# Optimization experiments

Hardware: AMD Instinct MI355X
Metric: run time of the kernel (lower is better)

## Reference

```python
import jax, jax.numpy as jnp
import numpy as np

HIDDEN = 768
HEADS = 12
HEAD_DIM = HIDDEN // HEADS
LN_EPS = 1e-12


def setup_inputs() -> dict:
    key = jax.random.key(0)
    ks = jax.random.split(key, 12)
    B, Lq, Lk = 8, 512, 1024
    s = 0.02
    return {
        "query": jax.random.normal(ks[0], (B, Lq, HIDDEN), jnp.float32),
        "key": jax.random.normal(ks[1], (B, Lk, HIDDEN), jnp.float32),
        "value": jax.random.normal(ks[2], (B, Lk, HIDDEN), jnp.float32),
        "attention_mask": jnp.zeros((B, 1, 1, Lk), jnp.float32),
        "q_attention_mask": jnp.zeros((B, 1, 1, Lq), jnp.float32),
        "Wq": jax.random.normal(ks[3], (HIDDEN, HIDDEN), jnp.float32) * s,
        "bq": jnp.zeros((HIDDEN,), jnp.float32),
        "Wk": jax.random.normal(ks[4], (HIDDEN, HIDDEN), jnp.float32) * s,
        "bk": jnp.zeros((HIDDEN,), jnp.float32),
        "Wv": jax.random.normal(ks[5], (HIDDEN, HIDDEN), jnp.float32) * s,
        "bv": jnp.zeros((HIDDEN,), jnp.float32),
        "Wo": jax.random.normal(ks[6], (HIDDEN, HIDDEN), jnp.float32) * s,
        "bo": jnp.zeros((HIDDEN,), jnp.float32),
        "ln_gamma": jnp.ones((HIDDEN,), jnp.float32),
        "ln_beta": jnp.zeros((HIDDEN,), jnp.float32),
    }


def _split_heads(x):  # [B, L, H*D] -> [B, H, L, D]
    B, L, _ = x.shape
    return x.reshape(B, L, HEADS, HEAD_DIM).transpose(0, 2, 1, 3)


def reference(query, key, value, attention_mask, q_attention_mask,
              Wq, bq, Wk, bk, Wv, bv, Wo, bo, ln_gamma, ln_beta):
    # QKV projections (dropout is identity at inference)
    q = _split_heads(query @ Wq.T + bq)   # [B,H,Lq,D]
    k = _split_heads(key @ Wk.T + bk)     # [B,H,Lk,D]
    v = _split_heads(value @ Wv.T + bv)   # [B,H,Lk,D]

    scores = jnp.einsum("bhqd,bhkd->bhqk", q, k) / jnp.sqrt(
        jnp.asarray(HEAD_DIM, q.dtype))
    scores = scores + attention_mask  # additive mask broadcast [B,1,1,Lk]
    probs = jax.nn.softmax(scores, axis=-1)
    ctx = jnp.einsum("bhqk,bhkd->bhqd", probs, v)  # [B,H,Lq,D]
    B, H, Lq, D = ctx.shape
    ctx = ctx.transpose(0, 2, 1, 3).reshape(B, Lq, H * D)

    # BertSelfOutput: dense + residual + LayerNorm
    h = ctx @ Wo.T + bo + query
    mu = jnp.mean(h, axis=-1, keepdims=True)
    var = jnp.mean(jnp.square(h - mu), axis=-1, keepdims=True)
    out = (h - mu) / jnp.sqrt(var + LN_EPS) * ln_gamma + ln_beta
    return out, probs
```

## Files before the change

kernel.cpp:

```cpp
#include <hip/hip_runtime.h>
#include <math.h>

#define HIDDEN 768
#define NHEADS 12
#define DHEAD  64
#define NB     8
#define LQ     512
#define LK     1024
#define LN_EPS 1e-12f
#define TS     1032

typedef __attribute__((ext_vector_type(8))) short short8;
typedef __attribute__((ext_vector_type(4))) float floatx4;

#define GLDS16(gp, lp) __builtin_amdgcn_global_load_lds( \
    (const __attribute__((address_space(1))) void*)(gp), \
    (__attribute__((address_space(3))) void*)(lp), 16, 0, 0)

__device__ __forceinline__ short f2bf(float f) {
    unsigned u = __float_as_uint(f);
    u = u + 0x7FFFu + ((u >> 16) & 1u);
    return (short)(u >> 16);
}

__device__ __forceinline__ float bf2f(short s) {
    return __uint_as_float(((unsigned)(unsigned short)s) << 16);
}

__global__ __launch_bounds__(256)
void cvt_f32_bf16(const float* __restrict__ in, short* __restrict__ out, int n4)
{
    int i = blockIdx.x * 256 + threadIdx.x;
    if (i >= n4) return;
    float4 v = ((const float4*)in)[i];
    short4 o;
    o.x = f2bf(v.x); o.y = f2bf(v.y); o.z = f2bf(v.z); o.w = f2bf(v.w);
    ((short4*)out)[i] = o;
}

__global__ __launch_bounds__(256)
void gemm_nt_mfma(const short* __restrict__ A, const short* __restrict__ B,
                  float* __restrict__ Cf, short* __restrict__ Cb,
                  const float* __restrict__ bias, const float* __restrict__ res,
                  int K, int lda, int ldb, int ldc, float alpha)
{
    __shared__ short As[4096];
    __shared__ short Bs[4096];

    int n0 = blockIdx.x * 128;
    int m0 = blockIdx.y * 128;
    int t    = threadIdx.x;
    int lane = t & 63, wave = t >> 6;
    int quad = lane >> 4, l15 = lane & 15;
    int wr = wave >> 1, wc = wave & 1;

    int e0 = t, e1 = 256 + t;
    int r0 = e0 >> 2, c0 = (e0 & 3) ^ ((r0 >> 1) & 3);
    int r1 = e1 >> 2, c1 = (e1 & 3) ^ ((r1 >> 1) & 3);
    const short* Ap0 = A + (size_t)(m0 + r0) * lda + c0 * 8;
    const short* Ap1 = A + (size_t)(m0 + r1) * lda + c1 * 8;
    const short* Bp0 = B + (size_t)(n0 + r0) * ldb + c0 * 8;
    const short* Bp1 = B + (size_t)(n0 + r1) * ldb + c1 * 8;

    int aoff[4], boff[4];
#pragma unroll
    for (int i = 0; i < 4; i++) {
        int ra = wr * 64 + i * 16 + l15;
        aoff[i] = (ra * 4 + (quad ^ ((ra >> 1) & 3))) * 8;
        int rb = wc * 64 + i * 16 + l15;
        boff[i] = (rb * 4 + (quad ^ ((rb >> 1) & 3))) * 8;
    }

    floatx4 acc[4][4] = {};

    for (int k0 = 0; k0 < K; k0 += 32) {
        GLDS16(Ap0, &As[e0 * 8]);
        GLDS16(Ap1, &As[e1 * 8]);
        GLDS16(Bp0, &Bs[e0 * 8]);
        GLDS16(Bp1, &Bs[e1 * 8]);
        Ap0 += 32; Ap1 += 32; Bp0 += 32; Bp1 += 32;
        __syncthreads();

        short8 af[4], bfr[4];
#pragma unroll
        for (int i = 0; i < 4; i++) af[i]  = *(const short8*)&As[aoff[i]];
#pragma unroll
        for (int j = 0; j < 4; j++) bfr[j] = *(const short8*)&Bs[boff[j]];
#pragma unroll
        for (int i = 0; i < 4; i++)
#pragma unroll
            for (int j = 0; j < 4; j++)
                acc[i][j] = __builtin_amdgcn_mfma_f32_16x16x32_bf16(
                    af[i], bfr[j], acc[i][j], 0, 0, 0);
        __syncthreads();
    }

#pragma unroll
    for (int i = 0; i < 4; i++) {
        int mb = m0 + wr * 64 + i * 16 + quad * 4;
#pragma unroll
        for (int j = 0; j < 4; j++) {
            int n = n0 + wc * 64 + j * 16 + l15;
            float bv = bias ? bias[n] : 0.f;
#pragma unroll
            for (int r = 0; r < 4; r++) {
                int m = mb + r;
                float v = alpha * acc[i][j][r] + bv;
                if (res) v += res[(size_t)m * ldc + n];
                if (Cb) Cb[(size_t)m * ldc + n] = f2bf(v);
                else    Cf[(size_t)m * ldc + n] = v;
            }
        }
    }
}

__global__ __launch_bounds__(256)
void transpose_v(const short* __restrict__ vb, short* __restrict__ vt)
{
    __shared__ short T[256 * 72];
    int kt = blockIdx.x, bh = blockIdx.y;
    int b = bh / 12, h = bh - b * 12;
    int t = threadIdx.x;
    const short* src = vb + ((size_t)b * LK + kt * 256) * HIDDEN + h * DHEAD;
#pragma unroll
    for (int it = 0; it < 8; it++) {
        int s = it * 256 + t;
        int k = s >> 3, c = s & 7;
        *(short8*)&T[k * 72 + c * 8] =
            *(const short8*)&src[(size_t)k * HIDDEN + c * 8];
    }
    __syncthreads();
    short* dst = vt + (size_t)bh * DHEAD * LK + kt * 256;
#pragma unroll
    for (int it = 0; it < 8; it++) {
        int s = it * 256 + t;
        int d = s >> 5, kc = s & 31;
        short8 v;
#pragma unroll
        for (int i = 0; i < 8; i++) v[i] = T[(kc * 8 + i) * 72 + d];
        *(short8*)&dst[(size_t)d * LK + kc * 8] = v;
    }
}

__global__ __launch_bounds__(256)
void fused_attn(const short* __restrict__ qb, const short* __restrict__ kb,
                const short* __restrict__ vt, const float* __restrict__ amask,
                float* __restrict__ probs, short* __restrict__ ctxb)
{
    __shared__ short S[16 * TS];
    __shared__ short KV[8192];
    __shared__ float mpart[4][16];
    __shared__ float lrow[16];

    int flat = blockIdx.y * 32 + blockIdx.x;
    int jj   = flat >> 3;
    int bh   = (flat & 7) * 12 + jj % 12;
    int qt   = jj / 12;
    int b = bh / 12, h = bh - b * 12;
    int m0 = qt * 16;

    const short* Qg = qb + ((size_t)b * LQ + m0) * HIDDEN + h * DHEAD;
    const short* Kg = kb + (size_t)b * LK * HIDDEN + h * DHEAD;
    const short* Vg = vt + (size_t)bh * DHEAD * LK;
    const float* Mg = amask + (size_t)b * LK;
    float* Pg = probs + (size_t)bh * LQ * LK + (size_t)m0 * LK;
    short* Cg = ctxb + ((size_t)b * LQ + m0) * HIDDEN + h * DHEAD;

    int t = threadIdx.x;
    int lane = t & 63, w = t >> 6;
    int quad = lane >> 4, l15 = lane & 15;

#pragma unroll
    for (int I = 0; I < 4; I++) {
        int s = I * 256 + t;
        int r = s >> 3, cs = s & 7, c = cs ^ (r & 7);
        GLDS16(Kg + (size_t)r * HIDDEN + c * 8, &KV[s * 8]);
    }

    short8 af[2];
#pragma unroll
    for (int ks = 0; ks < 2; ks++)
        af[ks] = *(const short8*)&Qg[(size_t)l15 * HIDDEN + ks * 32 + quad * 8];

    float mx[4];
#pragma unroll
    for (int r = 0; r < 4; r++) mx[r] = -3.0e38f;

    const float SC  = 0.125f * 1.44269504089f;
    const float L2E = 1.44269504089f;

    for (int kc = 0; kc < 8; kc++) {
        __syncthreads();
        floatx4 acc[2] = {};
#pragma unroll
        for (int ks = 0; ks < 2; ks++)
#pragma unroll
            for (int j = 0; j < 2; j++) {
                int rK = w * 32 + j * 16 + l15;
                int cs = (ks * 4 + quad) ^ (rK & 7);
                short8 bfr = *(const short8*)&KV[(rK * 8 + cs) * 8];
                acc[j] = __builtin_amdgcn_mfma_f32_16x16x32_bf16(
                    af[ks], bfr, acc[j], 0, 0, 0);
            }
        __syncthreads();
        if (kc < 7) {
            const short* Kn = Kg + (size_t)(kc + 1) * 128 * HIDDEN;
#pragma unroll
            for (int I = 0; I < 4; I++) {
                int s = I * 256 + t;
                int r = s >> 3, cs = s & 7, c = cs ^ (r & 7);
                GLDS16(Kn + (size_t)r * HIDDEN + c * 8, &KV[s * 8]);
            }
        }
#pragma unroll
        for (int j = 0; j < 2; j++) {
            int n = kc * 128 + w * 32 + j * 16 + l15;
            float mk = Mg[n] * L2E;
#pragma unroll
            for (int r = 0; r < 4; r++) {
                int m = quad * 4 + r;
                float v = acc[j][r] * SC + mk;
                S[m * TS + n] = f2bf(v);
                mx[r] = fmaxf(mx[r], v);
            }
        }
    }

#pragma unroll
    for (int d = 1; d < 16; d <<= 1)
#pragma unroll
        for (int r = 0; r < 4; r++)
            mx[r] = fmaxf(mx[r], __shfl_xor(mx[r], d));
    if (l15 == 0)
#pragma unroll
        for (int r = 0; r < 4; r++)
            mpart[w][quad * 4 + r] = mx[r];
    __syncthreads();

#pragma unroll
    for (int I = 0; I < 4; I++) {
        int s = I * 256 + t;
        int n = s >> 4, cs = s & 15, c = cs ^ (n & 15);
        GLDS16(Vg + (size_t)n * LK + c * 8, &KV[s * 8]);
    }

    {
        int r = t >> 4, seg = t & 15;
        float mr = fmaxf(fmaxf(mpart[0][r], mpart[1][r]),
                         fmaxf(mpart[2][r], mpart[3][r]));
        float sum = 0.f;
#pragma unroll
        for (int i = 0; i < 8; i++) {
            int u = i * 16 + seg;
            short8 v = *(const short8*)&S[r * TS + u * 8];
            short8 o;
#pragma unroll
            for (int e = 0; e < 8; e++) {
                float f = exp2f(bf2f(v[e]) - mr);
                o[e] = f2bf(f);
                sum += f;
            }
            *(short8*)&S[r * TS + u * 8] = o;
        }
        sum += __shfl_xor(sum, 1);
        sum += __shfl_xor(sum, 2);
        sum += __shfl_xor(sum, 4);
        sum += __shfl_xor(sum, 8);
        if (seg == 0) lrow[r] = sum;
    }

    floatx4 accO = {};
    for (int kc = 0; kc < 8; kc++) {
        __syncthreads();
#pragma unroll
        for (int ks = 0; ks < 4; ks++) {
            short8 pa = *(const short8*)&S[l15 * TS + kc * 128
                                           + ks * 32 + quad * 8];
            int n = w * 16 + l15;
            int cs = (ks * 4 + quad) ^ (n & 15);
            short8 bfr = *(const short8*)&KV[(n * 16 + cs) * 8];
            accO = __builtin_amdgcn_mfma_f32_16x16x32_bf16(
                pa, bfr, accO, 0, 0, 0);
        }
        __syncthreads();
        if (kc < 7) {
            const short* Vn = Vg + (kc + 1) * 128;
#pragma unroll
            for (int I = 0; I < 4; I++) {
                int s = I * 256 + t;
                int n = s >> 4, cs = s & 15, c = cs ^ (n & 15);
                GLDS16(Vn + (size_t)n * LK + c * 8, &KV[s * 8]);
            }
        }
#pragma unroll
        for (int rr = 0; rr < 2; rr++) {
            int r = kc * 2 + rr;
            float inv = 1.0f / lrow[r];
            short4 v = *(const short4*)&S[r * TS + t * 4];
            floatx4 o;
            o.x = bf2f(v.x) * inv; o.y = bf2f(v.y) * inv;
            o.z = bf2f(v.z) * inv; o.w = bf2f(v.w) * inv;
            __builtin_nontemporal_store(
                o, (floatx4*)(Pg + (size_t)r * LK) + t);
        }
    }

    int n = w * 16 + l15;
#pragma unroll
    for (int r = 0; r < 4; r++) {
        int m = quad * 4 + r;
        Cg[(size_t)m * HIDDEN + n] = f2bf(accO[r] / lrow[m]);
    }
}

__global__ __launch_bounds__(256)
void layernorm_rows(const float* __restrict__ H, const float* __restrict__ gamma,
                    const float* __restrict__ beta, float* __restrict__ out)
{
    int row = blockIdx.x;
    const float* h = H + (long)row * HIDDEN;
    int t = threadIdx.x;

    float x[3];
    float s = 0.f, ss = 0.f;
#pragma unroll
    for (int i = 0; i < 3; i++) {
        x[i] = h[t + 256 * i];
        s  += x[i];
        ss += x[i] * x[i];
    }
#pragma unroll
    for (int off = 32; off > 0; off >>= 1) {
        s  += __shfl_down(s, off);
        ss += __shfl_down(ss, off);
    }
    __shared__ float sh_s[4], sh_ss[4];
    int wave = t >> 6;
    if ((t & 63) == 0) { sh_s[wave] = s; sh_ss[wave] = ss; }
    __syncthreads();
    float S  = sh_s[0] + sh_s[1] + sh_s[2] + sh_s[3];
    float SS = sh_ss[0] + sh_ss[1] + sh_ss[2] + sh_ss[3];

    float mu  = S * (1.0f / HIDDEN);
    float var = SS * (1.0f / HIDDEN) - mu * mu;
    float inv = rsqrtf(var + LN_EPS);

    float* o = out + (long)row * HIDDEN;
#pragma unroll
    for (int i = 0; i < 3; i++) {
        int c = t + 256 * i;
        o[c] = (x[i] - mu) * inv * gamma[c] + beta[c];
    }
}

extern "C" void kernel_launch(void* const* d_in, const int* in_sizes, int n_in,
                              void* d_out, int out_size, void* d_ws, size_t ws_size,
                              hipStream_t stream)
{
    const float* query = (const float*)d_in[0];
    const float* key   = (const float*)d_in[1];
    const float* value = (const float*)d_in[2];
    const float* amask = (const float*)d_in[3];
    const float* Wq    = (const float*)d_in[5];
    const float* bq    = (const float*)d_in[6];
    const float* Wk    = (const float*)d_in[7];
    const float* bk    = (const float*)d_in[8];
    const float* Wv    = (const float*)d_in[9];
    const float* bv    = (const float*)d_in[10];
    const float* Wo    = (const float*)d_in[11];
    const float* bo    = (const float*)d_in[12];
    const float* gamma = (const float*)d_in[13];
    const float* beta  = (const float*)d_in[14];

    short* qx = (short*)d_ws;
    short* kx = qx + (long)4096 * 768;
    short* vx = kx + (long)8192 * 768;
    short* wq = vx + (long)8192 * 768;
    short* wk = wq + (long)768 * 768;
    short* wv = wk + (long)768 * 768;
    short* wo = wv + (long)768 * 768;
    short* qb = wo + (long)768 * 768;
    short* kb = qb + (long)4096 * 768;
    short* vb = kb + (long)8192 * 768;
    short* ctxb = qx;
    short* vt   = kx;
    float* hbuf = (float*)vx;

    float* out0  = (float*)d_out;
    float* probs = out0 + (long)NB * LQ * HIDDEN;

    cvt_f32_bf16<<<(4096 * 768 / 4 + 255) / 256, 256, 0, stream>>>(query, qx, 4096 * 768 / 4);
    cvt_f32_bf16<<<(8192 * 768 / 4 + 255) / 256, 256, 0, stream>>>(key,   kx, 8192 * 768 / 4);
    cvt_f32_bf16<<<(8192 * 768 / 4 + 255) / 256, 256, 0, stream>>>(value, vx, 8192 * 768 / 4);
    cvt_f32_bf16<<<(768 * 768 / 4 + 255) / 256, 256, 0, stream>>>(Wq, wq, 768 * 768 / 4);
    cvt_f32_bf16<<<(768 * 768 / 4 + 255) / 256, 256, 0, stream>>>(Wk, wk, 768 * 768 / 4);
    cvt_f32_bf16<<<(768 * 768 / 4 + 255) / 256, 256, 0, stream>>>(Wv, wv, 768 * 768 / 4);
    cvt_f32_bf16<<<(768 * 768 / 4 + 255) / 256, 256, 0, stream>>>(Wo, wo, 768 * 768 / 4);

    gemm_nt_mfma<<<dim3(6, 32), 256, 0, stream>>>(
        qx, wq, nullptr, qb, bq, nullptr, HIDDEN, HIDDEN, HIDDEN, HIDDEN, 1.0f);
    gemm_nt_mfma<<<dim3(6, 64), 256, 0, stream>>>(
        kx, wk, nullptr, kb, bk, nullptr, HIDDEN, HIDDEN, HIDDEN, HIDDEN, 1.0f);
    gemm_nt_mfma<<<dim3(6, 64), 256, 0, stream>>>(
        vx, wv, nullptr, vb, bv, nullptr, HIDDEN, HIDDEN, HIDDEN, HIDDEN, 1.0f);

    transpose_v<<<dim3(4, 96), 256, 0, stream>>>(vb, vt);

    fused_attn<<<dim3(32, 96), 256, 0, stream>>>(qb, kb, vt, amask, probs, ctxb);

    gemm_nt_mfma<<<dim3(6, 32), 256, 0, stream>>>(
        ctxb, wo, hbuf, nullptr, bo, query, HIDDEN, HIDDEN, HIDDEN, HIDDEN, 1.0f);

    layernorm_rows<<<NB * LQ, 256, 0, stream>>>(hbuf, gamma, beta, out0);
}
```

Before: 476.5 us.

## Merge conversion and QKV GEMM launches, double-buffer GEMM LDS loads

All seven fp32-to-bf16 conversions now run in one launch, and the three QKV projection GEMMs run in one grid that dispatches per block-row. The GEMM core now double-buffers its LDS tiles, issuing the next K-step's global-to-LDS loads before the current step's MFMAs and dropping one barrier per iteration. This cuts launch overhead, fills the device better for the small Q GEMM, and overlaps memory with compute. The cost is doubled LDS per block, which may lower occupancy, and a single barrier per step, which relies on the async-load ordering being safe.

```diff
diff --git a/kernel.cpp b/kernel.cpp
--- a/kernel.cpp
+++ b/kernel.cpp
@@ -28,27 +28,40 @@
 }
 
 __global__ __launch_bounds__(256)
-void cvt_f32_bf16(const float* __restrict__ in, short* __restrict__ out, int n4)
-{
-    int i = blockIdx.x * 256 + threadIdx.x;
-    if (i >= n4) return;
-    float4 v = ((const float4*)in)[i];
+void cvt_all(const float* __restrict__ q, const float* __restrict__ k,
+             const float* __restrict__ v,
+             const float* __restrict__ Wq, const float* __restrict__ Wk,
+             const float* __restrict__ Wv, const float* __restrict__ Wo,
+             short* __restrict__ dq, short* __restrict__ dk,
+             short* __restrict__ dv,
+             short* __restrict__ dwq, short* __restrict__ dwk,
+             short* __restrict__ dwv, short* __restrict__ dwo)
+{
+    int bx = blockIdx.x;
+    const float* src; short* dst; int base;
+    if (bx < 3072)       { src = q; dst = dq; base = bx; }
+    else if (bx < 9216)  { src = k; dst = dk; base = bx - 3072; }
+    else if (bx < 15360) { src = v; dst = dv; base = bx - 9216; }
+    else {
+        int wb = bx - 15360, wsel = wb / 576;
+        base = wb - wsel * 576;
+        src = (wsel == 0) ? Wq : (wsel == 1) ? Wk : (wsel == 2) ? Wv : Wo;
+        dst = (wsel == 0) ? dwq : (wsel == 1) ? dwk : (wsel == 2) ? dwv : dwo;
+    }
+    int i = base * 256 + threadIdx.x;
+    float4 vv = ((const float4*)src)[i];
     short4 o;
-    o.x = f2bf(v.x); o.y = f2bf(v.y); o.z = f2bf(v.z); o.w = f2bf(v.w);
-    ((short4*)out)[i] = o;
-}
-
-__global__ __launch_bounds__(256)
-void gemm_nt_mfma(const short* __restrict__ A, const short* __restrict__ B,
-                  float* __restrict__ Cf, short* __restrict__ Cb,
-                  const float* __restrict__ bias, const float* __restrict__ res,
-                  int K, int lda, int ldb, int ldc, float alpha)
-{
-    __shared__ short As[4096];
-    __shared__ short Bs[4096];
-
-    int n0 = blockIdx.x * 128;
-    int m0 = blockIdx.y * 128;
+    o.x = f2bf(vv.x); o.y = f2bf(vv.y); o.z = f2bf(vv.z); o.w = f2bf(vv.w);
+    ((short4*)dst)[i] = o;
+}
+
+__device__ __forceinline__ void gemm_core(
+    short (*As)[4096], short (*Bs)[4096],
+    const short* __restrict__ A, const short* __restrict__ B,
+    float* Cf, short* Cb,
+    const float* bias, const float* res,
+    int m0, int n0, int K, int lda, int ldb, int ldc, float alpha)
+{
     int t    = threadIdx.x;
     int lane = t & 63, wave = t >> 6;
     int quad = lane >> 4, l15 = lane & 15;
@@ -72,27 +85,35 @@
     }
 
     floatx4 acc[4][4] = {};
-
-    for (int k0 = 0; k0 < K; k0 += 32) {
-        GLDS16(Ap0, &As[e0 * 8]);
-        GLDS16(Ap1, &As[e1 * 8]);
-        GLDS16(Bp0, &Bs[e0 * 8]);
-        GLDS16(Bp1, &Bs[e1 * 8]);
-        Ap0 += 32; Ap1 += 32; Bp0 += 32; Bp1 += 32;
+    int nsteps = K >> 5;
+
+    GLDS16(Ap0, &As[0][e0 * 8]);
+    GLDS16(Ap1, &As[0][e1 * 8]);
+    GLDS16(Bp0, &Bs[0][e0 * 8]);
+    GLDS16(Bp1, &Bs[0][e1 * 8]);
+    Ap0 += 32; Ap1 += 32; Bp0 += 32; Bp1 += 32;
+
+    for (int s = 0; s < nsteps; s++) {
+        int cur = s & 1;
         __syncthreads();
-
+        if (s + 1 < nsteps) {
+            GLDS16(Ap0, &As[cur ^ 1][e0 * 8]);
+            GLDS16(Ap1, &As[cur ^ 1][e1 * 8]);
+            GLDS16(Bp0, &Bs[cur ^ 1][e0 * 8]);
+            GLDS16(Bp1, &Bs[cur ^ 1][e1 * 8]);
+            Ap0 += 32; Ap1 += 32; Bp0 += 32; Bp1 += 32;
+        }
         short8 af[4], bfr[4];
 #pragma unroll
-        for (int i = 0; i < 4; i++) af[i]  = *(const short8*)&As[aoff[i]];
-#pragma unroll
-        for (int j = 0; j < 4; j++) bfr[j] = *(const short8*)&Bs[boff[j]];
+        for (int i = 0; i < 4; i++) af[i]  = *(const short8*)&As[cur][aoff[i]];
+#pragma unroll
+        for (int j = 0; j < 4; j++) bfr[j] = *(const short8*)&Bs[cur][boff[j]];
 #pragma unroll
         for (int i = 0; i < 4; i++)
 #pragma unroll
             for (int j = 0; j < 4; j++)
                 acc[i][j] = __builtin_amdgcn_mfma_f32_16x16x32_bf16(
                     af[i], bfr[j], acc[i][j], 0, 0, 0);
-        __syncthreads();
     }
 
 #pragma unroll
@@ -112,6 +133,39 @@
             }
         }
     }
+}
+
+__global__ __launch_bounds__(256)
+void gemm_nt_mfma(const short* __restrict__ A, const short* __restrict__ B,
+                  float* __restrict__ Cf, short* __restrict__ Cb,
+                  const float* __restrict__ bias, const float* __restrict__ res,
+                  int K, int lda, int ldb, int ldc, float alpha)
+{
+    __shared__ short As[2][4096];
+    __shared__ short Bs[2][4096];
+    gemm_core(As, Bs, A, B, Cf, Cb, bias, res,
+              blockIdx.y * 128, blockIdx.x * 128, K, lda, ldb, ldc, alpha);
+}
+
+__global__ __launch_bounds__(256)
+void qkv_gemm(const short* __restrict__ qx, const short* __restrict__ kx,
+              const short* __restrict__ vx,
+              const short* __restrict__ wq, const short* __restrict__ wk,
+              const short* __restrict__ wv,
+              const float* __restrict__ bq, const float* __restrict__ bk,
+              const float* __restrict__ bv,
+              short* __restrict__ qb, short* __restrict__ kb,
+              short* __restrict__ vb)
+{
+    __shared__ short As[2][4096];
+    __shared__ short Bs[2][4096];
+    int yb = blockIdx.y;
+    const short *A, *B; const float* bias; short* C; int m0;
+    if (yb < 32)      { A = qx; B = wq; bias = bq; C = qb; m0 = yb * 128; }
+    else if (yb < 96) { A = kx; B = wk; bias = bk; C = kb; m0 = (yb - 32) * 128; }
+    else              { A = vx; B = wv; bias = bv; C = vb; m0 = (yb - 96) * 128; }
+    gemm_core(As, Bs, A, B, nullptr, C, bias, nullptr,
+              m0, blockIdx.x * 128, HIDDEN, HIDDEN, HIDDEN, HIDDEN, 1.0f);
 }
 
 __global__ __launch_bounds__(256)
@@ -389,20 +443,11 @@
     float* out0  = (float*)d_out;
     float* probs = out0 + (long)NB * LQ * HIDDEN;
 
-    cvt_f32_bf16<<<(4096 * 768 / 4 + 255) / 256, 256, 0, stream>>>(query, qx, 4096 * 768 / 4);
-    cvt_f32_bf16<<<(8192 * 768 / 4 + 255) / 256, 256, 0, stream>>>(key,   kx, 8192 * 768 / 4);
-    cvt_f32_bf16<<<(8192 * 768 / 4 + 255) / 256, 256, 0, stream>>>(value, vx, 8192 * 768 / 4);
-    cvt_f32_bf16<<<(768 * 768 / 4 + 255) / 256, 256, 0, stream>>>(Wq, wq, 768 * 768 / 4);
-    cvt_f32_bf16<<<(768 * 768 / 4 + 255) / 256, 256, 0, stream>>>(Wk, wk, 768 * 768 / 4);
-    cvt_f32_bf16<<<(768 * 768 / 4 + 255) / 256, 256, 0, stream>>>(Wv, wv, 768 * 768 / 4);
-    cvt_f32_bf16<<<(768 * 768 / 4 + 255) / 256, 256, 0, stream>>>(Wo, wo, 768 * 768 / 4);
-
-    gemm_nt_mfma<<<dim3(6, 32), 256, 0, stream>>>(
-        qx, wq, nullptr, qb, bq, nullptr, HIDDEN, HIDDEN, HIDDEN, HIDDEN, 1.0f);
-    gemm_nt_mfma<<<dim3(6, 64), 256, 0, stream>>>(
-        kx, wk, nullptr, kb, bk, nullptr, HIDDEN, HIDDEN, HIDDEN, HIDDEN, 1.0f);
-    gemm_nt_mfma<<<dim3(6, 64), 256, 0, stream>>>(
-        vx, wv, nullptr, vb, bv, nullptr, HIDDEN, HIDDEN, HIDDEN, HIDDEN, 1.0f);
+    cvt_all<<<17664, 256, 0, stream>>>(query, key, value, Wq, Wk, Wv, Wo,
+                                       qx, kx, vx, wq, wk, wv, wo);
+
+    qkv_gemm<<<dim3(6, 160), 256, 0, stream>>>(
+        qx, kx, vx, wq, wk, wv, bq, bk, bv, qb, kb, vb);
 
     transpose_v<<<dim3(4, 96), 256, 0, stream>>>(vb, vt);
 
```

Result: faster. 436.4 us (-8.4%).
